# Kernel optimization log

Hardware: AMD Instinct MI355X
Metric: run time of the kernel (lower is better)

Reference implementation:

```python
import jax, jax.numpy as jnp
import numpy as np


def setup_inputs() -> dict:
    key = jax.random.key(0)
    k1, k2 = jax.random.split(key)
    B, N, M, D = 16, 2048, 2048, 3
    predictions = jax.random.normal(k1, (B, N, D), dtype=jnp.float32)
    targets = jax.random.normal(k2, (B, M, D), dtype=jnp.float32)
    return {"predictions": predictions, "targets": targets}


def reference(predictions, targets):
    # Batched pairwise squared distances: [B, N, M]
    # d(i,j) = |x_i|^2 + |y_j|^2 - 2 x_i . y_j
    xx = jnp.sum(predictions * predictions, axis=-1)  # [B, N]
    yy = jnp.sum(targets * targets, axis=-1)          # [B, M]
    xy = jnp.einsum("bnd,bmd->bnm", predictions, targets)  # [B, N, M]
    P = xx[:, :, None] + yy[:, None, :] - 2.0 * xy    # [B, N, M]
    # Chamfer: sum of per-point nearest-neighbor squared distances, both directions
    loss = jnp.sum(jnp.min(P, axis=2)) + jnp.sum(jnp.min(P, axis=1))
    return loss
```

## Files before the change

kernel.cpp:

```cpp
#include <hip/hip_runtime.h>
#include <math.h>


typedef float v2f __attribute__((ext_vector_type(2)));

#define NPTS   2048
#define NCOMBO 32
#define SRCB   64
#define SPT    8
#define NQ     32
#define OPPT   (NPTS/NQ)
#define NBLK   (NCOMBO * 32)
#define PAD(i) ((i) + (((i) >> 6) << 2))

__device__ __forceinline__ v2f pkfma(v2f a, v2f b, v2f c) {
#if __has_builtin(__builtin_elementwise_fma)
    return __builtin_elementwise_fma(a, b, c);
#else
    v2f d; d.x = fmaf(a.x, b.x, c.x); d.y = fmaf(a.y, b.y, c.y); return d;
#endif
}

__global__ __launch_bounds__(256, 2) void chamfer_fused(
    const float* __restrict__ preds,
    const float* __restrict__ tgts,
    float* __restrict__ bsum)
{
    __shared__ __align__(16) float qx[2176];
    __shared__ __align__(16) float qy[2176];
    __shared__ __align__(16) float qz[2176];
    __shared__ __align__(16) float qw[2176];
    __shared__ float sm[4 * SRCB];

    const int combo = blockIdx.x & (NCOMBO - 1);
    const int chunk = blockIdx.x >> 5;
    const int dir   = combo >> 4;
    const int b     = combo & 15;

    const float* src = (dir ? tgts : preds) + (size_t)b * NPTS * 3;
    const float* opp = (dir ? preds : tgts) + (size_t)b * NPTS * 3;

    const float4* opp4 = (const float4*)opp;
    #pragma unroll
    for (int p = 0; p < 2; p++) {
        const int t  = threadIdx.x + 256 * p;
        const float4 A = opp4[3 * t + 0];
        const float4 B = opp4[3 * t + 1];
        const float4 C = opp4[3 * t + 2];
        const int i0 = 4 * t;
        {   const int pi = PAD(i0 + 0);
            qx[pi] = A.x; qy[pi] = A.y; qz[pi] = A.z;
            qw[pi] = A.x * A.x + A.y * A.y + A.z * A.z; }
        {   const int pi = PAD(i0 + 1);
            qx[pi] = A.w; qy[pi] = B.x; qz[pi] = B.y;
            qw[pi] = A.w * A.w + B.x * B.x + B.y * B.y; }
        {   const int pi = PAD(i0 + 2);
            qx[pi] = B.z; qy[pi] = B.w; qz[pi] = C.x;
            qw[pi] = B.z * B.z + B.w * B.w + C.x * C.x; }
        {   const int pi = PAD(i0 + 3);
            qx[pi] = C.y; qy[pi] = C.z; qz[pi] = C.w;
            qw[pi] = C.y * C.y + C.z * C.z + C.w * C.w; }
    }

    const int q = threadIdx.x >> 3;
    const int c = threadIdx.x & 7;

    float4 S[6];
    {
        const float4* s4 = (const float4*)(src + 3 * (chunk * SRCB + c * SPT));
        #pragma unroll
        for (int j = 0; j < 6; j++) S[j] = s4[j];
    }
    const float* sf = (const float*)S;

    v2f nn0[SPT], nn1[SPT], nn2[SPT];
    float m[SPT];
    #pragma unroll
    for (int k = 0; k < SPT; k++) {
        const float a0 = -2.0f * sf[3 * k + 0];
        const float a1 = -2.0f * sf[3 * k + 1];
        const float a2 = -2.0f * sf[3 * k + 2];
        nn0[k] = (v2f){a0, a0};
        nn1[k] = (v2f){a1, a1};
        nn2[k] = (v2f){a2, a2};
        m[k]   = INFINITY;
    }
    __syncthreads();

    const int base = q * 68;
    #pragma unroll 1
    for (int g = 0; g < OPPT / 4; g++) {
        const float4 X = *(const float4*)&qx[base + 4 * g];
        const float4 Y = *(const float4*)&qy[base + 4 * g];
        const float4 Z = *(const float4*)&qz[base + 4 * g];
        const float4 W = *(const float4*)&qw[base + 4 * g];
        const v2f Xa = {X.x, X.y}, Xb = {X.z, X.w};
        const v2f Ya = {Y.x, Y.y}, Yb = {Y.z, Y.w};
        const v2f Za = {Z.x, Z.y}, Zb = {Z.z, Z.w};
        const v2f Wa = {W.x, W.y}, Wb = {W.z, W.w};
        #pragma unroll
        for (int k = 0; k < SPT; k++) {
            const v2f sa = pkfma(nn0[k], Xa, pkfma(nn1[k], Ya, pkfma(nn2[k], Za, Wa)));
            m[k] = fminf(fminf(m[k], sa.x), sa.y);
            const v2f sb = pkfma(nn0[k], Xb, pkfma(nn1[k], Yb, pkfma(nn2[k], Zb, Wb)));
            m[k] = fminf(fminf(m[k], sb.x), sb.y);
        }
    }

    #pragma unroll
    for (int k = 0; k < SPT; k++) {
        float v = m[k];
        v = fminf(v, __shfl_xor(v, 8, 64));
        v = fminf(v, __shfl_xor(v, 16, 64));
        v = fminf(v, __shfl_xor(v, 32, 64));
        m[k] = v;
    }
    const int lane = threadIdx.x & 63;
    const int wid  = threadIdx.x >> 6;
    if (lane < 8) {
        #pragma unroll
        for (int k = 0; k < SPT; k++)
            sm[wid * SRCB + c * SPT + k] = m[k];
    }
    __syncthreads();

    if (threadIdx.x < 64) {
        const int off = (threadIdx.x & 7) * SPT + (threadIdx.x >> 3);
        float mn = fminf(fminf(sm[off],            sm[SRCB + off]),
                         fminf(sm[2 * SRCB + off], sm[3 * SRCB + off]));
        const int s = chunk * SRCB + off;
        const float x0 = src[3 * s + 0];
        const float x1 = src[3 * s + 1];
        const float x2 = src[3 * s + 2];
        float val = x0 * x0 + x1 * x1 + x2 * x2 + mn;
        #pragma unroll
        for (int o = 32; o > 0; o >>= 1)
            val += __shfl_down(val, o, 64);
        if (threadIdx.x == 0) bsum[blockIdx.x] = val;
    }
}

__global__ __launch_bounds__(256) void chamfer_sum(
    const float* __restrict__ bsum,
    float* __restrict__ out)
{
    __shared__ float wsum[4];

    float val = bsum[threadIdx.x]         + bsum[threadIdx.x + 256]
              + bsum[threadIdx.x + 512]   + bsum[threadIdx.x + 768];

    #pragma unroll
    for (int o = 32; o > 0; o >>= 1)
        val += __shfl_down(val, o, 64);

    const int lane = threadIdx.x & 63;
    const int wid  = threadIdx.x >> 6;
    if (lane == 0) wsum[wid] = val;
    __syncthreads();
    if (threadIdx.x == 0)
        out[0] = wsum[0] + wsum[1] + wsum[2] + wsum[3];
}

extern "C" void kernel_launch(void* const* d_in, const int* in_sizes, int n_in,
                              void* d_out, int out_size, void* d_ws, size_t ws_size,
                              hipStream_t stream) {
    const float* preds = (const float*)d_in[0];
    const float* tgts  = (const float*)d_in[1];
    float* out  = (float*)d_out;
    float* bsum = (float*)d_ws;

    chamfer_fused<<<NBLK, 256, 0, stream>>>(preds, tgts, bsum);
    chamfer_sum<<<1, 256, 0, stream>>>(bsum, out);
}
```

Baseline: 66.87 us.

## Retile chamfer inner loop to 16 sources per thread over 32 opposite points

Each thread now holds 16 source points, up from 8, and scans 32 opposite points instead of 64, so 4 threads share a source slice and 64 thread groups split the opposite set. This doubles the FMAs done per shared-memory load of X/Y/Z/W, cutting LDS traffic relative to compute. The launch-bound occupancy hint is raised to 3 blocks per CU. The extra register arrays could push register pressure against the higher occupancy target, and the cross-lane reduction gains one more shuffle stage.

Result: slower. 69.88 us (+4.5%).

```diff
diff --git a/kernel.cpp b/kernel.cpp
--- a/kernel.cpp
+++ b/kernel.cpp
@@ -7,9 +7,8 @@
 #define NPTS   2048
 #define NCOMBO 32
 #define SRCB   64
-#define SPT    8
-#define NQ     32
-#define OPPT   (NPTS/NQ)
+#define SPT    16
+#define OPPT   32
 #define NBLK   (NCOMBO * 32)
 #define PAD(i) ((i) + (((i) >> 6) << 2))
 
@@ -21,7 +20,7 @@
 #endif
 }
 
-__global__ __launch_bounds__(256, 2) void chamfer_fused(
+__global__ __launch_bounds__(256, 3) void chamfer_fused(
     const float* __restrict__ preds,
     const float* __restrict__ tgts,
     float* __restrict__ bsum)
@@ -62,32 +61,32 @@
             qw[pi] = C.y * C.y + C.z * C.z + C.w * C.w; }
     }
 
-    const int q = threadIdx.x >> 3;
-    const int c = threadIdx.x & 7;
-
-    float4 S[6];
-    {
-        const float4* s4 = (const float4*)(src + 3 * (chunk * SRCB + c * SPT));
-        #pragma unroll
-        for (int j = 0; j < 6; j++) S[j] = s4[j];
-    }
-    const float* sf = (const float*)S;
+    const int q = threadIdx.x >> 2;
+    const int c = threadIdx.x & 3;
 
     v2f nn0[SPT], nn1[SPT], nn2[SPT];
     float m[SPT];
+    const float4* s4 = (const float4*)(src + 3 * (chunk * SRCB + c * SPT));
     #pragma unroll
-    for (int k = 0; k < SPT; k++) {
-        const float a0 = -2.0f * sf[3 * k + 0];
-        const float a1 = -2.0f * sf[3 * k + 1];
-        const float a2 = -2.0f * sf[3 * k + 2];
-        nn0[k] = (v2f){a0, a0};
-        nn1[k] = (v2f){a1, a1};
-        nn2[k] = (v2f){a2, a2};
-        m[k]   = INFINITY;
+    for (int p = 0; p < 4; p++) {
+        const float4 A = s4[3 * p + 0];
+        const float4 B = s4[3 * p + 1];
+        const float4 C = s4[3 * p + 2];
+        const int k0 = 4 * p;
+        {   const float a0 = -2.0f * A.x, a1 = -2.0f * A.y, a2 = -2.0f * A.z;
+            nn0[k0+0] = (v2f){a0, a0}; nn1[k0+0] = (v2f){a1, a1}; nn2[k0+0] = (v2f){a2, a2}; }
+        {   const float a0 = -2.0f * A.w, a1 = -2.0f * B.x, a2 = -2.0f * B.y;
+            nn0[k0+1] = (v2f){a0, a0}; nn1[k0+1] = (v2f){a1, a1}; nn2[k0+1] = (v2f){a2, a2}; }
+        {   const float a0 = -2.0f * B.z, a1 = -2.0f * B.w, a2 = -2.0f * C.x;
+            nn0[k0+2] = (v2f){a0, a0}; nn1[k0+2] = (v2f){a1, a1}; nn2[k0+2] = (v2f){a2, a2}; }
+        {   const float a0 = -2.0f * C.y, a1 = -2.0f * C.z, a2 = -2.0f * C.w;
+            nn0[k0+3] = (v2f){a0, a0}; nn1[k0+3] = (v2f){a1, a1}; nn2[k0+3] = (v2f){a2, a2}; }
     }
+    #pragma unroll
+    for (int k = 0; k < SPT; k++) m[k] = INFINITY;
     __syncthreads();
 
-    const int base = q * 68;
+    const int base = PAD(q * 32);
     #pragma unroll 1
     for (int g = 0; g < OPPT / 4; g++) {
         const float4 X = *(const float4*)&qx[base + 4 * g];
@@ -110,6 +109,7 @@
     #pragma unroll
     for (int k = 0; k < SPT; k++) {
         float v = m[k];
+        v = fminf(v, __shfl_xor(v, 4, 64));
         v = fminf(v, __shfl_xor(v, 8, 64));
         v = fminf(v, __shfl_xor(v, 16, 64));
         v = fminf(v, __shfl_xor(v, 32, 64));
@@ -117,15 +117,15 @@
     }
     const int lane = threadIdx.x & 63;
     const int wid  = threadIdx.x >> 6;
-    if (lane < 8) {
+    if (lane < 4) {
         #pragma unroll
         for (int k = 0; k < SPT; k++)
-            sm[wid * SRCB + c * SPT + k] = m[k];
+            sm[wid * SRCB + lane * SPT + k] = m[k];
     }
     __syncthreads();
 
     if (threadIdx.x < 64) {
-        const int off = (threadIdx.x & 7) * SPT + (threadIdx.x >> 3);
+        const int off = threadIdx.x;
         float mn = fminf(fminf(sm[off],            sm[SRCB + off]),
                          fminf(sm[2 * SRCB + off], sm[3 * SRCB + off]));
         const int s = chunk * SRCB + off;
```
